# Performance work log

Hardware: AMD Instinct MI355X
Metric: run time of the kernel (lower is better)

## Reference

```python
import jax, jax.numpy as jnp
import numpy as np

NEG_INF = -9e15  # matches torch's -9000000000000000.0 mask value
ALPHA = 0.2      # LeakyReLU negative slope


def setup_inputs() -> dict:
    key = jax.random.key(0)
    k1, k2, k3, k4 = jax.random.split(key, 4)
    B, N, Fin, Fout, H = 32, 512, 256, 64, 8
    x = jax.random.normal(k1, (B, N, Fin), dtype=jnp.float32)
    adj = (jax.random.uniform(k2, (B, N, N)) < 0.5).astype(jnp.float32)
    # W: Linear(in_features, out_features*n_heads, bias=False) weight, stored as (Fin, Fout*H)
    W = jax.random.normal(k3, (Fin, Fout * H), dtype=jnp.float32) / np.sqrt(Fin).astype(np.float32)
    # a: attention vector per head over concat(src,dst) features -> (H, 2*Fout)
    a = jax.random.normal(k4, (H, 2 * Fout), dtype=jnp.float32) * 0.1
    return {"x": x, "adj": adj, "W": W, "a": a}


def reference(x, adj, W, a):
    # x: (B,N,Fin), adj: (B,N,N), W: (Fin, H*F), a: (H, 2F)
    B, N, _ = x.shape
    H, twoF = a.shape
    F = twoF // 2
    h = (x @ W).reshape(B, N, H, F)  # (B,N,H,F)
    # Decompose concat-score: e_ij = lrelu(h_i . a_src + h_j . a_dst) -- same math
    # as (cat(h_i,h_j) * a).sum(-1) without materializing (B,N,N,H,2F).
    s_src = jnp.einsum('bnhf,hf->bnh', h, a[:, :F])  # (B,N,H)
    s_dst = jnp.einsum('bnhf,hf->bnh', h, a[:, F:])  # (B,N,H)
    e = s_src[:, :, None, :] + s_dst[:, None, :, :]  # (B,N,N,H)
    e = jax.nn.leaky_relu(e, negative_slope=ALPHA)
    e = jnp.where(adj[..., None] > 0, e, NEG_INF)
    attn = jax.nn.softmax(e, axis=2)  # softmax over neighbors j (dim=2)
    # dropout omitted (eval mode / p effectively 0 for the reference baseline)
    h_prime = jnp.einsum('bijh,bjhf->bihf', attn, h)  # (B,N,H,F)
    return h_prime.reshape(B, N, H * F)  # concat=True
```

## Files before the change

kernel.cpp:

```cpp
#include <hip/hip_runtime.h>
#include <hip/hip_bf16.h>


#define ALPHA  0.2f
#define ESCALE 1.4426950408889634f

typedef __bf16 bf16x8 __attribute__((ext_vector_type(8)));
typedef __bf16 bf16x4 __attribute__((ext_vector_type(4)));
typedef float  f32x4  __attribute__((ext_vector_type(4)));

#if __has_builtin(__builtin_amdgcn_exp2f)
#define EXP2(x) __builtin_amdgcn_exp2f(x)
#else
#define EXP2(x) exp2f(x)
#endif

#define HT_STRIDE 520
#define WT_STRIDE 264

struct Smem {
    __bf16 hT[64][HT_STRIDE];
    __bf16 WT[64][WT_STRIDE];
    float  E[512], G[512], F[512], H[512];
    float  asrc[64], adst[64];
};

__device__ inline bf16x8 ld8(const float* p) {
    float4 a0 = *(const float4*)p;
    float4 a1 = *(const float4*)(p + 4);
    bf16x8 r;
    r[0]=(__bf16)a0.x; r[1]=(__bf16)a0.y; r[2]=(__bf16)a0.z; r[3]=(__bf16)a0.w;
    r[4]=(__bf16)a1.x; r[5]=(__bf16)a1.y; r[6]=(__bf16)a1.z; r[7]=(__bf16)a1.w;
    return r;
}

__global__ __launch_bounds__(512) void k_pack(const float* __restrict__ adj,
                                              unsigned int* __restrict__ mask) {
    const int i = blockIdx.x, b = blockIdx.y;
    const int tid = threadIdx.x, wave = tid >> 6, lane = tid & 63;
    float v = adj[((long)b * 512 + i) * 512 + tid];
    unsigned long long m = __ballot(v > 0.f);
    if (lane == 0) {
        mask[(b * 16 + 2 * wave) * 512 + i]     = (unsigned int)m;
        mask[(b * 16 + 2 * wave + 1) * 512 + i] = (unsigned int)(m >> 32);
    }
}

template <bool USEM>
__global__ __launch_bounds__(512, 1) void k_gat(const float* __restrict__ x,
                                                const float* __restrict__ adj,
                                                const unsigned int* __restrict__ mask,
                                                const float* __restrict__ W,
                                                const float* __restrict__ a,
                                                float* __restrict__ out) {
    __shared__ Smem sm;
    const int b = blockIdx.x, h = blockIdx.y;
    const int tid  = threadIdx.x;
    const int wave = tid >> 6, lane = tid & 63;
    const int quad = lane >> 4, col = lane & 15;

    if (tid < 128) {
        float v = a[h * 128 + tid] * ESCALE;
        if (tid < 64) sm.asrc[tid] = v; else sm.adst[tid - 64] = v;
    }
    {
        int c = tid & 63, k0 = tid >> 6;
        #pragma unroll 4
        for (int t = 0; t < 32; ++t)
            sm.WT[c][k0 + t * 8] = (__bf16)W[(long)(k0 + t * 8) * 512 + h * 64 + c];
    }
    __syncthreads();

    {
        const float* xb = x + (long)b * 512 * 256;
        f32x4 acc[4][4] = {};
        for (int ks = 0; ks < 8; ++ks) {
            int k0 = ks * 32 + quad * 8;
            bf16x8 av[4], bv[4];
            #pragma unroll
            for (int it = 0; it < 4; ++it)
                av[it] = ld8(xb + (long)(wave * 64 + it * 16 + col) * 256 + k0);
            #pragma unroll
            for (int nt = 0; nt < 4; ++nt)
                bv[nt] = *(const bf16x8*)(&sm.WT[nt * 16 + col][k0]);
            #pragma unroll
            for (int it = 0; it < 4; ++it)
                #pragma unroll
                for (int nt = 0; nt < 4; ++nt)
                    acc[it][nt] = __builtin_amdgcn_mfma_f32_16x16x32_bf16(av[it], bv[nt], acc[it][nt], 0, 0, 0);
        }
        #pragma unroll
        for (int it = 0; it < 4; ++it)
            #pragma unroll
            for (int nt = 0; nt < 4; ++nt) {
                int f = nt * 16 + col;
                int j = wave * 64 + it * 16 + quad * 4;
                bf16x4 pk = { (__bf16)acc[it][nt][0], (__bf16)acc[it][nt][1],
                              (__bf16)acc[it][nt][2], (__bf16)acc[it][nt][3] };
                *(bf16x4*)(&sm.hT[f][j]) = pk;
            }
    }
    __syncthreads();

    {
        float as = 0.f, ad = 0.f;
        #pragma unroll 8
        for (int f = 0; f < 64; ++f) {
            float v = (float)sm.hT[f][tid];
            as += v * sm.asrc[f];
            ad += v * sm.adst[f];
        }
        sm.E[tid] = EXP2(as);
        sm.G[tid] = EXP2(ALPHA * as);
        sm.F[tid] = EXP2(ad);
        sm.H[tid] = EXP2(ALPHA * ad);
    }
    __syncthreads();

    {
        const int qs = quad * 8;
        float EI[4], GI[4];
        int iw[4];
        const float* arow[4];
        #pragma unroll
        for (int it = 0; it < 4; ++it) {
            int i = wave * 64 + it * 16 + col;
            iw[it] = i;
            EI[it] = sm.E[i];
            GI[it] = sm.G[i];
            if (!USEM) arow[it] = adj + ((long)b * 512 + i) * 512;
        }
        const unsigned int* mbase = mask + (long)b * 16 * 512;
        bf16x8 ones;
        #pragma unroll
        for (int u = 0; u < 8; ++u) ones[u] = (__bf16)1.0f;

        f32x4 acc[4][4] = {};
        f32x4 accs[4]   = {};
        unsigned int pm[4];
        float4 pa0[4], pa1[4];
        #pragma unroll
        for (int it = 0; it < 4; ++it) {
            if (USEM) pm[it] = mbase[iw[it]];
            else {
                pa0[it] = *(const float4*)(arow[it] + qs);
                pa1[it] = *(const float4*)(arow[it] + qs + 4);
            }
        }
        for (int ks = 0; ks < 16; ++ks) {
            int j0 = ks * 32 + qs;
            unsigned int cm[4];
            float am[4][8];
            #pragma unroll
            for (int it = 0; it < 4; ++it) {
                if (USEM) cm[it] = pm[it];
                else {
                    am[it][0]=pa0[it].x; am[it][1]=pa0[it].y;
                    am[it][2]=pa0[it].z; am[it][3]=pa0[it].w;
                    am[it][4]=pa1[it].x; am[it][5]=pa1[it].y;
                    am[it][6]=pa1[it].z; am[it][7]=pa1[it].w;
                }
            }
            if (ks < 15) {
                #pragma unroll
                for (int it = 0; it < 4; ++it) {
                    if (USEM) pm[it] = mbase[(ks + 1) * 512 + iw[it]];
                    else {
                        pa0[it] = *(const float4*)(arow[it] + j0 + 32);
                        pa1[it] = *(const float4*)(arow[it] + j0 + 36);
                    }
                }
            }
            f32x4 F0 = *(const f32x4*)&sm.F[j0];
            f32x4 F1 = *(const f32x4*)&sm.F[j0 + 4];
            f32x4 H0 = *(const f32x4*)&sm.H[j0];
            f32x4 H1 = *(const f32x4*)&sm.H[j0 + 4];
            float Fv[8] = {F0[0],F0[1],F0[2],F0[3],F1[0],F1[1],F1[2],F1[3]};
            float Hv[8] = {H0[0],H0[1],H0[2],H0[3],H1[0],H1[1],H1[2],H1[3]};
            bf16x8 P[4];
            #pragma unroll
            for (int it = 0; it < 4; ++it)
                #pragma unroll
                for (int u = 0; u < 8; ++u) {
                    float ef = EI[it] * Fv[u];
                    float gh = GI[it] * Hv[u];
                    float sel = ef > 1.0f ? ef : gh;
                    float p;
                    if (USEM) p = ((cm[it] >> (qs + u)) & 1u) ? sel : 0.0f;
                    else      p = sel * am[it][u];
                    P[it][u] = (__bf16)p;
                }
            bf16x8 bv[4];
            #pragma unroll
            for (int nt = 0; nt < 4; ++nt)
                bv[nt] = *(const bf16x8*)(&sm.hT[nt * 16 + col][j0]);
            #pragma unroll
            for (int it = 0; it < 4; ++it) {
                #pragma unroll
                for (int nt = 0; nt < 4; ++nt)
                    acc[it][nt] = __builtin_amdgcn_mfma_f32_16x16x32_bf16(P[it], bv[nt], acc[it][nt], 0, 0, 0);
                accs[it] = __builtin_amdgcn_mfma_f32_16x16x32_bf16(P[it], ones, accs[it], 0, 0, 0);
            }
        }
        #pragma unroll
        for (int it = 0; it < 4; ++it)
            #pragma unroll
            for (int r = 0; r < 4; ++r) {
                float s = accs[it][r];
                float inv = (s > 0.f) ? 1.0f / s : 0.f;
                int i = wave * 64 + it * 16 + quad * 4 + r;
                float* orow = out + ((long)b * 512 + i) * 512 + h * 64;
                #pragma unroll
                for (int nt = 0; nt < 4; ++nt)
                    orow[nt * 16 + col] = acc[it][nt][r] * inv;
            }
    }
}

extern "C" void kernel_launch(void* const* d_in, const int* in_sizes, int n_in,
                              void* d_out, int out_size, void* d_ws, size_t ws_size,
                              hipStream_t stream) {
    const float* x   = (const float*)d_in[0];
    const float* adj = (const float*)d_in[1];
    const float* W   = (const float*)d_in[2];
    const float* a   = (const float*)d_in[3];
    float* out = (float*)d_out;

    const size_t MASK_BYTES = 32u * 16u * 512u * 4u;
    if (ws_size >= MASK_BYTES) {
        unsigned int* mask = (unsigned int*)d_ws;
        k_pack<<<dim3(512, 32), 512, 0, stream>>>(adj, mask);
        k_gat<true><<<dim3(32, 8), 512, 0, stream>>>(x, adj, mask, W, a, out);
    } else {
        k_gat<false><<<dim3(32, 8), 512, 0, stream>>>(x, adj, nullptr, W, a, out);
    }
}
```

Measured before the change: 144.0 us.

## Split GAT rows across two blocks and pretranspose W globally to raise occupancy

Splits each (batch, head) block into two blocks over the query rows, so the grid doubles to 512 blocks with half the accumulators per wave. W's bf16 transpose moves out of shared memory into a separate prep kernel, which shrinks LDS use and raises the launch bound to allow 4 blocks. The goal is more concurrent blocks on the many CUs and less idle time. In exchange, each of the two half-blocks recomputes the full x@W projection and the score vectors for its (batch, head), doubling that work, and an extra kernel launch is added.

```diff
diff --git a/kernel.cpp b/kernel.cpp
--- a/kernel.cpp
+++ b/kernel.cpp
@@ -16,11 +16,9 @@
 #endif
 
 #define HT_STRIDE 520
-#define WT_STRIDE 264
 
 struct Smem {
     __bf16 hT[64][HT_STRIDE];
-    __bf16 WT[64][WT_STRIDE];
     float  E[512], G[512], F[512], H[512];
     float  asrc[64], adst[64];
 };
@@ -46,15 +44,23 @@
     }
 }
 
-template <bool USEM>
-__global__ __launch_bounds__(512, 1) void k_gat(const float* __restrict__ x,
+__global__ __launch_bounds__(512) void k_prep(const float* __restrict__ W,
+                                              __bf16* __restrict__ WTg) {
+    int t = blockIdx.x * 512 + threadIdx.x;
+    int c = t & 511, k = t >> 9;
+    WTg[c * 256 + k] = (__bf16)W[k * 512 + c];
+}
+
+template <bool PRE>
+__global__ __launch_bounds__(512, 4) void k_gat(const float* __restrict__ x,
                                                 const float* __restrict__ adj,
                                                 const unsigned int* __restrict__ mask,
+                                                const __bf16* __restrict__ WTg,
                                                 const float* __restrict__ W,
                                                 const float* __restrict__ a,
                                                 float* __restrict__ out) {
     __shared__ Smem sm;
-    const int b = blockIdx.x, h = blockIdx.y;
+    const int b = blockIdx.x, h = blockIdx.y, ihalf = blockIdx.z;
     const int tid  = threadIdx.x;
     const int wave = tid >> 6, lane = tid & 63;
     const int quad = lane >> 4, col = lane & 15;
@@ -63,16 +69,10 @@
         float v = a[h * 128 + tid] * ESCALE;
         if (tid < 64) sm.asrc[tid] = v; else sm.adst[tid - 64] = v;
     }
-    {
-        int c = tid & 63, k0 = tid >> 6;
-        #pragma unroll 4
-        for (int t = 0; t < 32; ++t)
-            sm.WT[c][k0 + t * 8] = (__bf16)W[(long)(k0 + t * 8) * 512 + h * 64 + c];
-    }
-    __syncthreads();
 
     {
         const float* xb = x + (long)b * 512 * 256;
+        const __bf16* wg = WTg + (long)h * 64 * 256;
         f32x4 acc[4][4] = {};
         for (int ks = 0; ks < 8; ++ks) {
             int k0 = ks * 32 + quad * 8;
@@ -81,8 +81,15 @@
             for (int it = 0; it < 4; ++it)
                 av[it] = ld8(xb + (long)(wave * 64 + it * 16 + col) * 256 + k0);
             #pragma unroll
-            for (int nt = 0; nt < 4; ++nt)
-                bv[nt] = *(const bf16x8*)(&sm.WT[nt * 16 + col][k0]);
+            for (int nt = 0; nt < 4; ++nt) {
+                if (PRE) {
+                    bv[nt] = *(const bf16x8*)(wg + (nt * 16 + col) * 256 + k0);
+                } else {
+                    #pragma unroll
+                    for (int u = 0; u < 8; ++u)
+                        bv[nt][u] = (__bf16)W[(long)(k0 + u) * 512 + h * 64 + nt * 16 + col];
+                }
+            }
             #pragma unroll
             for (int it = 0; it < 4; ++it)
                 #pragma unroll
@@ -119,29 +126,29 @@
 
     {
         const int qs = quad * 8;
-        float EI[4], GI[4];
-        int iw[4];
-        const float* arow[4];
-        #pragma unroll
-        for (int it = 0; it < 4; ++it) {
-            int i = wave * 64 + it * 16 + col;
+        float EI[2], GI[2];
+        int iw[2];
+        const float* arow[2];
+        #pragma unroll
+        for (int it = 0; it < 2; ++it) {
+            int i = ihalf * 256 + wave * 32 + it * 16 + col;
             iw[it] = i;
             EI[it] = sm.E[i];
             GI[it] = sm.G[i];
-            if (!USEM) arow[it] = adj + ((long)b * 512 + i) * 512;
+            if (!PRE) arow[it] = adj + ((long)b * 512 + i) * 512;
         }
         const unsigned int* mbase = mask + (long)b * 16 * 512;
         bf16x8 ones;
         #pragma unroll
         for (int u = 0; u < 8; ++u) ones[u] = (__bf16)1.0f;
 
-        f32x4 acc[4][4] = {};
-        f32x4 accs[4]   = {};
-        unsigned int pm[4];
-        float4 pa0[4], pa1[4];
-        #pragma unroll
-        for (int it = 0; it < 4; ++it) {
-            if (USEM) pm[it] = mbase[iw[it]];
+        f32x4 acc[2][4] = {};
+        f32x4 accs[2]   = {};
+        unsigned int pm[2];
+        float4 pa0[2], pa1[2];
+        #pragma unroll
+        for (int it = 0; it < 2; ++it) {
+            if (PRE) pm[it] = mbase[iw[it]];
             else {
                 pa0[it] = *(const float4*)(arow[it] + qs);
                 pa1[it] = *(const float4*)(arow[it] + qs + 4);
@@ -149,11 +156,11 @@
         }
         for (int ks = 0; ks < 16; ++ks) {
             int j0 = ks * 32 + qs;
-            unsigned int cm[4];
-            float am[4][8];
-            #pragma unroll
-            for (int it = 0; it < 4; ++it) {
-                if (USEM) cm[it] = pm[it];
+            unsigned int cm[2];
+            float am[2][8];
+            #pragma unroll
+            for (int it = 0; it < 2; ++it) {
+                if (PRE) cm[it] = pm[it];
                 else {
                     am[it][0]=pa0[it].x; am[it][1]=pa0[it].y;
                     am[it][2]=pa0[it].z; am[it][3]=pa0[it].w;
@@ -163,8 +170,8 @@
             }
             if (ks < 15) {
                 #pragma unroll
-                for (int it = 0; it < 4; ++it) {
-                    if (USEM) pm[it] = mbase[(ks + 1) * 512 + iw[it]];
+                for (int it = 0; it < 2; ++it) {
+                    if (PRE) pm[it] = mbase[(ks + 1) * 512 + iw[it]];
                     else {
                         pa0[it] = *(const float4*)(arow[it] + j0 + 32);
                         pa1[it] = *(const float4*)(arow[it] + j0 + 36);
@@ -177,17 +184,17 @@
             f32x4 H1 = *(const f32x4*)&sm.H[j0 + 4];
             float Fv[8] = {F0[0],F0[1],F0[2],F0[3],F1[0],F1[1],F1[2],F1[3]};
             float Hv[8] = {H0[0],H0[1],H0[2],H0[3],H1[0],H1[1],H1[2],H1[3]};
-            bf16x8 P[4];
-            #pragma unroll
-            for (int it = 0; it < 4; ++it)
+            bf16x8 P[2];
+            #pragma unroll
+            for (int it = 0; it < 2; ++it)
                 #pragma unroll
                 for (int u = 0; u < 8; ++u) {
                     float ef = EI[it] * Fv[u];
                     float gh = GI[it] * Hv[u];
                     float sel = ef > 1.0f ? ef : gh;
                     float p;
-                    if (USEM) p = ((cm[it] >> (qs + u)) & 1u) ? sel : 0.0f;
-                    else      p = sel * am[it][u];
+                    if (PRE) p = ((cm[it] >> (qs + u)) & 1u) ? sel : 0.0f;
+                    else     p = sel * am[it][u];
                     P[it][u] = (__bf16)p;
                 }
             bf16x8 bv[4];
@@ -195,7 +202,7 @@
             for (int nt = 0; nt < 4; ++nt)
                 bv[nt] = *(const bf16x8*)(&sm.hT[nt * 16 + col][j0]);
             #pragma unroll
-            for (int it = 0; it < 4; ++it) {
+            for (int it = 0; it < 2; ++it) {
                 #pragma unroll
                 for (int nt = 0; nt < 4; ++nt)
                     acc[it][nt] = __builtin_amdgcn_mfma_f32_16x16x32_bf16(P[it], bv[nt], acc[it][nt], 0, 0, 0);
@@ -203,12 +210,12 @@
             }
         }
         #pragma unroll
-        for (int it = 0; it < 4; ++it)
+        for (int it = 0; it < 2; ++it)
             #pragma unroll
             for (int r = 0; r < 4; ++r) {
                 float s = accs[it][r];
                 float inv = (s > 0.f) ? 1.0f / s : 0.f;
-                int i = wave * 64 + it * 16 + quad * 4 + r;
+                int i = ihalf * 256 + wave * 32 + it * 16 + quad * 4 + r;
                 float* orow = out + ((long)b * 512 + i) * 512 + h * 64;
                 #pragma unroll
                 for (int nt = 0; nt < 4; ++nt)
@@ -227,11 +234,14 @@
     float* out = (float*)d_out;
 
     const size_t MASK_BYTES = 32u * 16u * 512u * 4u;
-    if (ws_size >= MASK_BYTES) {
+    const size_t WTG_BYTES  = 512u * 256u * 2u;
+    if (ws_size >= MASK_BYTES + WTG_BYTES) {
         unsigned int* mask = (unsigned int*)d_ws;
+        __bf16* WTg = (__bf16*)((char*)d_ws + MASK_BYTES);
         k_pack<<<dim3(512, 32), 512, 0, stream>>>(adj, mask);
-        k_gat<true><<<dim3(32, 8), 512, 0, stream>>>(x, adj, mask, W, a, out);
+        k_prep<<<256, 512, 0, stream>>>(W, WTg);
+        k_gat<true><<<dim3(32, 8, 2), 512, 0, stream>>>(x, adj, mask, WTg, W, a, out);
     } else {
-        k_gat<false><<<dim3(32, 8), 512, 0, stream>>>(x, adj, nullptr, W, a, out);
-    }
-}
+        k_gat<false><<<dim3(32, 8, 2), 512, 0, stream>>>(x, adj, nullptr, nullptr, W, a, out);
+    }
+}
```

After: 173.4 us. 20.4% more time.
